# Performance work log

Hardware: AMD Instinct MI355X
Metric: run time of the kernel (lower is better)

The kernel has to match this reference:

```python
import jax, jax.numpy as jnp
import numpy as np

B, C_IN, H, W = 4, 256, 64, 64
LATENT = 256


def setup_inputs() -> dict:
    key = jax.random.key(0)
    ks = jax.random.split(key, 12)
    s_in = 1.0 / np.sqrt(C_IN)
    s_lat = 1.0 / np.sqrt(LATENT)
    return {
        "x": jax.random.normal(ks[0], (B, C_IN, H, W), dtype=jnp.float32),
        # 1x1 conv weights stored as [out, in]
        "wq": jax.random.normal(ks[1], (LATENT, C_IN), dtype=jnp.float32) * s_in,
        "bq": jnp.zeros((LATENT,), dtype=jnp.float32),
        "wk": jax.random.normal(ks[2], (LATENT, C_IN), dtype=jnp.float32) * s_in,
        "bk": jnp.zeros((LATENT,), dtype=jnp.float32),
        "wv": jax.random.normal(ks[3], (LATENT, C_IN), dtype=jnp.float32) * s_in,
        "bv": jnp.zeros((LATENT,), dtype=jnp.float32),
        "w_out": jax.random.normal(ks[4], (C_IN, LATENT), dtype=jnp.float32) * s_lat,
        "b_out": jnp.zeros((C_IN,), dtype=jnp.float32),
        # positional-embedding MLP (torch nn.Linear: y = x @ W.T + b)
        "mlp_w1": jax.random.normal(ks[5], (LATENT, LATENT), dtype=jnp.float32) * s_lat,
        "mlp_b1": jnp.zeros((LATENT,), dtype=jnp.float32),
        "mlp_w2": jax.random.normal(ks[6], (LATENT, LATENT), dtype=jnp.float32) * s_lat,
        "mlp_b2": jnp.zeros((LATENT,), dtype=jnp.float32),
    }


def _sinusoidal_table(timesteps, dim):
    # embed[t, d] = sin(arg) if d even else cos(arg), arg = t / 10000**(2d/dim)
    t = jnp.arange(timesteps, dtype=jnp.float32)[:, None]
    p = jnp.arange(dim, dtype=jnp.float32)[None, :]
    w = t / jnp.power(jnp.float32(10000.0), 2.0 * p / dim)
    even = (jnp.arange(dim) % 2 == 0)[None, :]
    return jnp.where(even, jnp.sin(w), jnp.cos(w))  # [T, dim]


def _conv1x1(x, w, b):
    # x: [B, Cin, H, W], w: [Cout, Cin]
    return jnp.einsum('bchw,oc->bohw', x, w) + b[None, :, None, None]


def reference(x, wq, bq, wk, bk, wv, bv, w_out, b_out, mlp_w1, mlp_b1, mlp_w2, mlp_b2):
    batch, _, h, w_ = x.shape
    L = wq.shape[0]
    hw = h * w_

    q = _conv1x1(x, wq, bq)
    k = _conv1x1(x, wk, bk)
    v = _conv1x1(x, wv, bv)

    pe = _sinusoidal_table(hw, L)                     # [HW, L]
    pe = jax.nn.silu(pe @ mlp_w1.T + mlp_b1) @ mlp_w2.T + mlp_b2
    pe = pe.reshape(1, L, h, w_)                      # faithful to torch reshape

    q = (q + pe).reshape(batch, L, hw)
    k = (k + pe).reshape(batch, L, hw)
    v = (v + pe).reshape(batch, L, hw)

    # attention[b, i, j] = sum_c q[b, c, i] * k[b, c, j] / sqrt(L)
    att = jnp.einsum('bci,bcj->bij', q, k) / jnp.sqrt(jnp.float32(L))
    att = jax.nn.softmax(att, axis=1)                 # SAGAN-style: softmax over queries
    res = jnp.einsum('bci,bij->bcj', v, att)          # bmm(v, attention)
    res = res.reshape(batch, L, h, w_)
    return _conv1x1(res, w_out, b_out)
```

## Files before the change

kernel.cpp:

```cpp
#include <hip/hip_runtime.h>
#include <cstdint>


typedef short s8v __attribute__((ext_vector_type(8)));
typedef float f32x4 __attribute__((ext_vector_type(4)));
typedef unsigned int u32x2 __attribute__((ext_vector_type(2)));
typedef unsigned int u32x4 __attribute__((ext_vector_type(4)));

#define DEVI static __device__ __forceinline__

DEVI unsigned short f2bf(float f) {
  union { float f; uint32_t u; } x; x.f = f;
  uint32_t u = x.u;
  return (unsigned short)((u + 0x7fffu + ((u >> 16) & 1u)) >> 16);
}

DEVI void pl32swap(uint32_t& a, uint32_t& b) {
#if __has_builtin(__builtin_amdgcn_permlane32_swap)
  u32x2 r = __builtin_amdgcn_permlane32_swap(a, b, false, false);
  a = r[0]; b = r[1];
#else
  asm("v_permlane32_swap_b32 %0, %1" : "+v"(a), "+v"(b));
#endif
}

DEVI void gl_lds16(const void* g, void* l) {
  __builtin_amdgcn_global_load_lds(
      (const __attribute__((address_space(1))) void*)g,
      (__attribute__((address_space(3))) void*)l,
      16, 0, 0);
}

DEVI void stage(const unsigned short* src, int ld, unsigned short* lds, int t) {
  gl_lds16(src + (long)(t >> 2) * ld + (t & 3) * 8, lds + (t >> 6) * 512);
}

template <int OBF, int BIAS, int PEM, int SILU>
__global__ __launch_bounds__(256) void gemm_nt(
    const unsigned short* __restrict__ A, const unsigned short* __restrict__ B,
    void* __restrict__ Cp, int K, int N, int ld, long sA, long sB, long sC,
    const float* __restrict__ bias, const float* __restrict__ pe, float scale) {
  const int bz = blockIdx.z;
  const unsigned short* Ab = A + (long)bz * sA;
  const unsigned short* Bb = B + (long)bz * sB;
  const int m0 = blockIdx.x * 128, n0 = blockIdx.y * 128;
  __shared__ __align__(16) unsigned short As[4096], Bs[4096];
  const int t = threadIdx.x;
  const int wave = t >> 6, lane = t & 63;
  const int wr = wave >> 1, wc = wave & 1;

  f32x4 acc[4][4];
#pragma unroll
  for (int i = 0; i < 4; i++)
#pragma unroll
    for (int j = 0; j < 4; j++) acc[i][j] = f32x4{0.f, 0.f, 0.f, 0.f};

  const int rl = lane & 15, kp = (lane >> 4) * 8;

  for (int k0 = 0; k0 < K; k0 += 32) {
    stage(Ab + (long)m0 * ld + k0, ld, As, t);
    stage(Ab + (long)(m0 + 64) * ld + k0, ld, As + 2048, t);
    stage(Bb + (long)n0 * ld + k0, ld, Bs, t);
    stage(Bb + (long)(n0 + 64) * ld + k0, ld, Bs + 2048, t);
    __syncthreads();

    s8v af[4], bfr[4];
#pragma unroll
    for (int i = 0; i < 4; i++)
      af[i] = *(const s8v*)(As + (wr * 64 + i * 16 + rl) * 32 + kp);
#pragma unroll
    for (int j = 0; j < 4; j++)
      bfr[j] = *(const s8v*)(Bs + (wc * 64 + j * 16 + rl) * 32 + kp);
#pragma unroll
    for (int i = 0; i < 4; i++)
#pragma unroll
      for (int j = 0; j < 4; j++)
        acc[i][j] = __builtin_amdgcn_mfma_f32_16x16x32_bf16(af[i], bfr[j],
                                                            acc[i][j], 0, 0, 0);
    __syncthreads();
  }

  const long cb = (long)bz * sC;
#pragma unroll
  for (int i = 0; i < 4; i++) {
    const int r0 = m0 + wr * 64 + i * 16 + (lane >> 4) * 4;
#pragma unroll
    for (int j = 0; j < 4; j++) {
      const int col = n0 + wc * 64 + j * 16 + (lane & 15);
#pragma unroll
      for (int r = 0; r < 4; r++) {
        const int row = r0 + r;
        float val = acc[i][j][r] * scale;
        if (BIAS == 1) val += bias[row];
        if (BIAS == 2) val += bias[col];
        if (PEM == 1) val += pe[(long)row * 4096 + col];
        if (PEM == 2) val += pe[(long)col * 4096 + row];
        if (SILU) val = val / (1.0f + __expf(-val));
        const long ci = cb + (long)row * N + col;
        if (OBF)
          ((unsigned short*)Cp)[ci] = f2bf(val);
        else
          ((float*)Cp)[ci] = val;
      }
    }
  }
}

__global__ __launch_bounds__(256) void gemm_qk(
    const unsigned short* __restrict__ XT, const unsigned short* __restrict__ wqb,
    const unsigned short* __restrict__ wkb, unsigned short* __restrict__ qT,
    unsigned short* __restrict__ kT, const float* __restrict__ bq,
    const float* __restrict__ bk, const float* __restrict__ pe) {
  const int bz = blockIdx.z;
  const unsigned short* Ab = XT + (long)bz * 1048576;
  const int m0 = blockIdx.x * 128, n0 = blockIdx.y * 128;
  __shared__ __align__(16) unsigned short As[4096], Bq[4096], Bk[4096];
  const int t = threadIdx.x;
  const int wave = t >> 6, lane = t & 63;
  const int wr = wave >> 1, wc = wave & 1;

  f32x4 aq[4][4], ak[4][4];
#pragma unroll
  for (int i = 0; i < 4; i++)
#pragma unroll
    for (int j = 0; j < 4; j++) {
      aq[i][j] = f32x4{0.f, 0.f, 0.f, 0.f};
      ak[i][j] = f32x4{0.f, 0.f, 0.f, 0.f};
    }

  const int rl = lane & 15, kp = (lane >> 4) * 8;

  for (int k0 = 0; k0 < 256; k0 += 32) {
    stage(Ab + (long)m0 * 256 + k0, 256, As, t);
    stage(Ab + (long)(m0 + 64) * 256 + k0, 256, As + 2048, t);
    stage(wqb + (long)n0 * 256 + k0, 256, Bq, t);
    stage(wqb + (long)(n0 + 64) * 256 + k0, 256, Bq + 2048, t);
    stage(wkb + (long)n0 * 256 + k0, 256, Bk, t);
    stage(wkb + (long)(n0 + 64) * 256 + k0, 256, Bk + 2048, t);
    __syncthreads();

    s8v af[4], bq4[4], bk4[4];
#pragma unroll
    for (int i = 0; i < 4; i++)
      af[i] = *(const s8v*)(As + (wr * 64 + i * 16 + rl) * 32 + kp);
#pragma unroll
    for (int j = 0; j < 4; j++) {
      bq4[j] = *(const s8v*)(Bq + (wc * 64 + j * 16 + rl) * 32 + kp);
      bk4[j] = *(const s8v*)(Bk + (wc * 64 + j * 16 + rl) * 32 + kp);
    }
#pragma unroll
    for (int i = 0; i < 4; i++)
#pragma unroll
      for (int j = 0; j < 4; j++) {
        aq[i][j] = __builtin_amdgcn_mfma_f32_16x16x32_bf16(af[i], bq4[j],
                                                           aq[i][j], 0, 0, 0);
        ak[i][j] = __builtin_amdgcn_mfma_f32_16x16x32_bf16(af[i], bk4[j],
                                                           ak[i][j], 0, 0, 0);
      }
    __syncthreads();
  }

  const long cb = (long)bz * 1048576;
#pragma unroll
  for (int i = 0; i < 4; i++) {
    const int r0 = m0 + wr * 64 + i * 16 + (lane >> 4) * 4;
#pragma unroll
    for (int j = 0; j < 4; j++) {
      const int col = n0 + wc * 64 + j * 16 + (lane & 15);
#pragma unroll
      for (int r = 0; r < 4; r++) {
        const int row = r0 + r;
        const float p = pe[(long)col * 4096 + row];
        qT[cb + (long)row * 256 + col] = f2bf(aq[i][j][r] + bq[col] + p);
        kT[cb + (long)row * 256 + col] = f2bf(ak[i][j][r] + bk[col] + p);
      }
    }
  }
}

__global__ __launch_bounds__(512, 2) void flash_attn(
    const unsigned short* __restrict__ qTp, const unsigned short* __restrict__ kTp,
    const unsigned short* __restrict__ vBp, float* __restrict__ oPart,
    float* __restrict__ lPart) {
  const int bid = blockIdx.x;
  const int xcd = bid & 7;
  const int b = xcd >> 1, ihalf = xcd & 1;
  const int j0 = (bid >> 3) * 128;
  const long S = 1048576;
  const long ibase = (long)ihalf * 2048;
  const unsigned short* q = qTp + (long)b * S;
  const unsigned short* k = kTp + (long)b * S;
  const unsigned short* v = vBp + (long)b * S;
  const int ob = b * 2 + ihalf;

  __shared__ __align__(16) unsigned char ldsb[131584];

  const int t = threadIdx.x;
  const int wave = t >> 6, lane = t & 63;
  const int jq = wave & 3, ch = wave >> 2;
  const int rl = lane & 15, g = lane >> 4;
  const int kp = g * 8;
  const int ksw = ((g ^ ((rl >> 1) & 3)) << 3);
  const int qrow = (rl & 3) | ((rl & 4) << 1) | ((rl & 8) >> 1);
  const int kswq = ((g ^ ((qrow >> 1) & 3)) << 3);
  const int th = t >> 8, tt = t & 255;

  const unsigned short* krow = k + (long)(j0 + jq * 32 + rl) * 256 + kp;
  s8v kreg[2][8];
#pragma unroll
  for (int jf = 0; jf < 2; jf++)
#pragma unroll
    for (int s = 0; s < 8; s++)
      kreg[jf][s] = *(const s8v*)(krow + jf * 16 * 256 + s * 32);

  f32x4 oacc[16][2];
#pragma unroll
  for (int cf = 0; cf < 16; cf++)
#pragma unroll
    for (int jf = 0; jf < 2; jf++) oacc[cf][jf] = f32x4{0.f, 0.f, 0.f, 0.f};
  float plsum[2] = {0.f, 0.f};

  const int tr = tt >> 2, tc = tt & 3;
  const int sc = (tc ^ ((tr >> 1) & 3)) * 8;
  const unsigned short* qsrc[4];
  const unsigned short* vsrc[4];
  const int dsto = (tt >> 6) * 512;
#pragma unroll
  for (int ss = 0; ss < 4; ss++) {
    const int s_ = ss * 2 + th;
    qsrc[ss] = q + ibase * 256 + s_ * 32 + (long)tr * 256 + sc;
    vsrc[ss] = v + (long)((s_ >> 1) * 64) * 4096 + ibase + (s_ & 1) * 32 +
               (long)tr * 4096 + sc;
  }

#define STAGE_QV(bufsel)                                                     \
  {                                                                          \
    unsigned short* qD = (unsigned short*)(ldsb + ((bufsel) << 15));         \
    unsigned short* vD = (unsigned short*)(ldsb + 65536 + ((bufsel) << 15)); \
    _Pragma("unroll") for (int ss = 0; ss < 4; ss++) {                       \
      const int s_ = ss * 2 + th;                                            \
      gl_lds16(qsrc[ss], qD + s_ * 2048 + dsto);                             \
      gl_lds16(vsrc[ss], vD + s_ * 2048 + dsto);                             \
      qsrc[ss] += 16384;                     \
      vsrc[ss] += 64;                        \
    }                                                                        \
  }

  STAGE_QV(0)

  for (int n = 0; n < 32; ++n) {
    const int cur = n & 1;
    __syncthreads();
    STAGE_QV(cur ^ 1)

    f32x4 sa[2][2];
#pragma unroll
    for (int kk = 0; kk < 2; kk++)
#pragma unroll
      for (int jf = 0; jf < 2; jf++) sa[kk][jf] = f32x4{0.f, 0.f, 0.f, 0.f};
    const unsigned short* qbase =
        (const unsigned short*)(ldsb + (cur << 15)) +
        (ch * 32 + qrow) * 32 + kswq;
#pragma unroll
    for (int s = 0; s < 8; s++) {
      s8v qf0 = *(const s8v*)(qbase + s * 2048);
      s8v qf1 = *(const s8v*)(qbase + s * 2048 + 512);
      sa[0][0] = __builtin_amdgcn_mfma_f32_16x16x32_bf16(qf0, kreg[0][s],
                                                         sa[0][0], 0, 0, 0);
      sa[0][1] = __builtin_amdgcn_mfma_f32_16x16x32_bf16(qf0, kreg[1][s],
                                                         sa[0][1], 0, 0, 0);
      sa[1][0] = __builtin_amdgcn_mfma_f32_16x16x32_bf16(qf1, kreg[0][s],
                                                         sa[1][0], 0, 0, 0);
      sa[1][1] = __builtin_amdgcn_mfma_f32_16x16x32_bf16(qf1, kreg[1][s],
                                                         sa[1][1], 0, 0, 0);
    }

    uint32_t pd[2][2][2];
#pragma unroll
    for (int kk = 0; kk < 2; kk++)
#pragma unroll
      for (int jf = 0; jf < 2; jf++) {
        const float p0 = exp2f(sa[kk][jf][0] * 0.09016844005556021f);
        const float p1 = exp2f(sa[kk][jf][1] * 0.09016844005556021f);
        const float p2 = exp2f(sa[kk][jf][2] * 0.09016844005556021f);
        const float p3 = exp2f(sa[kk][jf][3] * 0.09016844005556021f);
        plsum[jf] += (p0 + p1) + (p2 + p3);
        pd[kk][jf][0] = (uint32_t)f2bf(p0) | ((uint32_t)f2bf(p1) << 16);
        pd[kk][jf][1] = (uint32_t)f2bf(p2) | ((uint32_t)f2bf(p3) << 16);
      }

    s8v pB[2];
#pragma unroll
    for (int jf = 0; jf < 2; jf++) {
      uint32_t a0 = pd[0][jf][0], b0 = pd[1][jf][0];
      uint32_t a1 = pd[0][jf][1], b1 = pd[1][jf][1];
      pl32swap(a0, b0);
      pl32swap(a1, b1);
      u32x4 w4 = {a0, a1, b0, b1};
      pB[jf] = __builtin_bit_cast(s8v, w4);
    }

    const unsigned short* vbase =
        (const unsigned short*)(ldsb + 65536 + (cur << 15)) + ch * 2048 +
        rl * 32 + ksw;
#pragma unroll
    for (int cf = 0; cf < 16; cf++) {
      s8v vb = *(const s8v*)(vbase + (cf >> 2) * 4096 + (cf & 3) * 512);
      oacc[cf][0] = __builtin_amdgcn_mfma_f32_16x16x32_bf16(vb, pB[0],
                                                            oacc[cf][0], 0, 0, 0);
      oacc[cf][1] = __builtin_amdgcn_mfma_f32_16x16x32_bf16(vb, pB[1],
                                                            oacc[cf][1], 0, 0, 0);
    }
  }

#pragma unroll
  for (int jf = 0; jf < 2; jf++) {
    plsum[jf] += __shfl_xor(plsum[jf], 16);
    plsum[jf] += __shfl_xor(plsum[jf], 32);
  }

  __syncthreads();
  float4* ex = (float4*)ldsb;
  float* exl = (float*)(ldsb + 131072);
  if (ch == 1) {
#pragma unroll
    for (int jf = 0; jf < 2; jf++) {
#pragma unroll
      for (int cf = 0; cf < 16; cf++)
        ex[jq * 2048 + (jf * 16 + rl) * 64 + cf * 4 + g] =
            float4{oacc[cf][jf][0], oacc[cf][jf][1], oacc[cf][jf][2],
                   oacc[cf][jf][3]};
      if (g == 0) exl[jq * 32 + jf * 16 + rl] = plsum[jf];
    }
  }
  __syncthreads();
  if (ch == 0) {
    float4* op4 = (float4*)(oPart + (long)ob * 1048576);
#pragma unroll
    for (int jf = 0; jf < 2; jf++) {
      const int jl = jq * 32 + jf * 16 + rl;
      if (g == 0)
        lPart[(long)ob * 4096 + j0 + jl] = plsum[jf] + exl[jl];
#pragma unroll
      for (int cf = 0; cf < 16; cf++) {
        const float4 o = ex[jq * 2048 + (jf * 16 + rl) * 64 + cf * 4 + g];
        op4[(long)(j0 + jl) * 64 + cf * 4 + g] =
            float4{oacc[cf][jf][0] + o.x, oacc[cf][jf][1] + o.y,
                   oacc[cf][jf][2] + o.z, oacc[cf][jf][3] + o.w};
      }
    }
  }
#undef STAGE_QV
}

__global__ __launch_bounds__(256) void combine_o(
    const float* __restrict__ oPart, const float* __restrict__ lPart,
    unsigned short* __restrict__ rT) {
  const long idx = (long)blockIdx.x * 256 + threadIdx.x;
  const int c4 = idx & 63;
  const int j = (idx >> 6) & 4095;
  const int b = idx >> 18;
  const long p0 = ((long)(b * 2) * 1048576 + (long)j * 256) / 4 + c4;
  const float4 a = ((const float4*)oPart)[p0];
  const float4 d = ((const float4*)oPart)[p0 + 262144];
  const float l = lPart[(long)(b * 2) * 4096 + j] +
                  lPart[(long)(b * 2 + 1) * 4096 + j];
  const float inv = 1.0f / l;
  ushort4 o;
  o.x = f2bf((a.x + d.x) * inv);
  o.y = f2bf((a.y + d.y) * inv);
  o.z = f2bf((a.z + d.z) * inv);
  o.w = f2bf((a.w + d.w) * inv);
  ((ushort4*)rT)[(long)b * 262144 + (long)j * 64 + c4] = o;
}

__global__ __launch_bounds__(256) void convert6(
    const float* __restrict__ a0, const float* __restrict__ a1,
    const float* __restrict__ a2, const float* __restrict__ a3,
    const float* __restrict__ a4, const float* __restrict__ a5,
    unsigned short* __restrict__ dst) {
  int idx = blockIdx.x * 256 + threadIdx.x;
  int m = idx >> 16, r = idx & 65535;
  const float* s;
  switch (m) {
    case 0: s = a0; break;
    case 1: s = a1; break;
    case 2: s = a2; break;
    case 3: s = a3; break;
    case 4: s = a4; break;
    default: s = a5; break;
  }
  dst[idx] = f2bf(s[r]);
}

__global__ __launch_bounds__(256) void embed_k(unsigned short* __restrict__ e) {
  int idx = blockIdx.x * 256 + threadIdx.x;
  int t = idx >> 8, d = idx & 255;
  float freq = powf(10000.0f, -(float)d * (1.0f / 128.0f));
  float w = (float)t * freq;
  float r = (d & 1) ? cosf(w) : sinf(w);
  e[idx] = f2bf(r);
}

__global__ void transpose_x(const float* __restrict__ x,
                            unsigned short* __restrict__ xt) {
  __shared__ float tile[32][33];
  const int b = blockIdx.z;
  const int s0 = blockIdx.x * 32, c0 = blockIdx.y * 32;
  const int tx = threadIdx.x, ty = threadIdx.y;
  const float* xb = x + (long)b * 256 * 4096;
#pragma unroll
  for (int r = 0; r < 32; r += 8)
    tile[ty + r][tx] = xb[(long)(c0 + ty + r) * 4096 + s0 + tx];
  __syncthreads();
  unsigned short* xtb = xt + (long)b * 4096 * 256;
#pragma unroll
  for (int r = 0; r < 32; r += 8)
    xtb[(long)(s0 + ty + r) * 256 + c0 + tx] = f2bf(tile[tx][ty + r]);
}

extern "C" void kernel_launch(void* const* d_in, const int* in_sizes, int n_in,
                              void* d_out, int out_size, void* d_ws,
                              size_t ws_size, hipStream_t stream) {
  const float* x  = (const float*)d_in[0];
  const float* wq = (const float*)d_in[1];
  const float* bq = (const float*)d_in[2];
  const float* wk = (const float*)d_in[3];
  const float* bk = (const float*)d_in[4];
  const float* wv = (const float*)d_in[5];
  const float* bv = (const float*)d_in[6];
  const float* wo = (const float*)d_in[7];
  const float* bo = (const float*)d_in[8];
  const float* w1 = (const float*)d_in[9];
  const float* b1 = (const float*)d_in[10];
  const float* w2 = (const float*)d_in[11];
  const float* b2 = (const float*)d_in[12];
  float* out = (float*)d_out;

  char* ws = (char*)d_ws;
  unsigned short* wqb = (unsigned short*)(ws + 0);
  unsigned short* wkb = (unsigned short*)(ws + 131072);
  unsigned short* wvb = (unsigned short*)(ws + 262144);
  unsigned short* wob = (unsigned short*)(ws + 393216);
  unsigned short* w1b = (unsigned short*)(ws + 524288);
  unsigned short* w2b = (unsigned short*)(ws + 655360);
  unsigned short* emb = (unsigned short*)(ws + 786432);
  unsigned short* h1b = (unsigned short*)(ws + 2883584);
  float*          peF = (float*)(ws + 4980736);
  unsigned short* XT  = (unsigned short*)(ws + 9175040);
  unsigned short* qT  = (unsigned short*)(ws + 17563648);
  unsigned short* kT  = (unsigned short*)(ws + 25952256);
  unsigned short* vB  = (unsigned short*)(ws + 34340864);
  unsigned short* rT  = (unsigned short*)(ws + 42729472);
  float*          oP  = (float*)(ws + 51118080);
  float*          lP  = (float*)(ws + 84672512);
  (void)ws_size; (void)in_sizes; (void)n_in; (void)out_size;

  const dim3 B256(256);
  const long S = 1048576;

  convert6<<<1536, B256, 0, stream>>>(wq, wk, wv, wo, w1, w2, wqb);
  embed_k<<<4096, B256, 0, stream>>>(emb);
  gemm_nt<1, 2, 0, 1><<<dim3(32, 2, 1), B256, 0, stream>>>(
      emb, w1b, h1b, 256, 256, 256, 0, 0, 0, b1, nullptr, 1.0f);
  gemm_nt<0, 2, 0, 0><<<dim3(32, 2, 1), B256, 0, stream>>>(
      h1b, w2b, peF, 256, 256, 256, 0, 0, 0, b2, nullptr, 1.0f);
  transpose_x<<<dim3(128, 8, 4), dim3(32, 8), 0, stream>>>(x, XT);
  gemm_qk<<<dim3(32, 2, 4), B256, 0, stream>>>(XT, wqb, wkb, qT, kT, bq, bk,
                                               peF);
  gemm_nt<1, 1, 1, 0><<<dim3(2, 32, 4), B256, 0, stream>>>(
      wvb, XT, vB, 256, 4096, 256, 0, S, S, bv, peF, 1.0f);

  flash_attn<<<256, dim3(512), 0, stream>>>(qT, kT, vB, oP, lP);
  combine_o<<<4096, B256, 0, stream>>>(oP, lP, rT);

  gemm_nt<0, 1, 0, 0><<<dim3(2, 32, 4), B256, 0, stream>>>(
      wob, rT, out, 256, 4096, 256, 0, S, S, bo, nullptr, 1.0f);
}
```

Measured before the change: 167.2 us.

## Fuse split-softmax combine into output projection GEMM and cheapen embedding math

Removes the separate combine_o kernel and the bf16 rT intermediate. The output 1x1-conv GEMM now reads the two fp32 partial attention outputs and their row sums directly, normalises them, converts to bf16 and writes its B tile to LDS. The sinusoidal embedding kernel also swaps powf/sinf/cosf for exp2f and __sincosf. In exchange, each GEMM block re-reads fp32 partials (twice the bytes of bf16) with no double buffering, and the fast sincos loses accuracy for large arguments.

```diff
diff --git a/kernel.cpp b/kernel.cpp
--- a/kernel.cpp
+++ b/kernel.cpp
@@ -178,6 +178,89 @@
   }
 }
 
+__global__ __launch_bounds__(256) void gemm_out_f(
+    const unsigned short* __restrict__ wob, const float* __restrict__ oPart,
+    const float* __restrict__ lPart, const float* __restrict__ bo,
+    float* __restrict__ out) {
+  const int bz = blockIdx.z;
+  const int m0 = blockIdx.x * 128, n0 = blockIdx.y * 128;
+  __shared__ __align__(16) unsigned short As[4096], Bs[4096];
+  const int t = threadIdx.x;
+  const int wave = t >> 6, lane = t & 63;
+  const int wr = wave >> 1, wc = wave & 1;
+
+  f32x4 acc[4][4];
+#pragma unroll
+  for (int i = 0; i < 4; i++)
+#pragma unroll
+    for (int j = 0; j < 4; j++) acc[i][j] = f32x4{0.f, 0.f, 0.f, 0.f};
+
+  const int rl = lane & 15, kp = (lane >> 4) * 8;
+  const int tr = t >> 2, tc8 = (t & 3) * 8;
+
+  const int j0_ = n0 + tr, j1_ = n0 + 64 + tr;
+  const float* l0p = lPart + (long)(bz * 2) * 4096;
+  const float* l1p = lPart + (long)(bz * 2 + 1) * 4096;
+  const float inv0 = 1.0f / (l0p[j0_] + l1p[j0_]);
+  const float inv1 = 1.0f / (l0p[j1_] + l1p[j1_]);
+  const float* oP0 = oPart + (long)(bz * 2) * 1048576;
+  const float* oP1 = oPart + (long)(bz * 2 + 1) * 1048576;
+
+  for (int k0 = 0; k0 < 256; k0 += 32) {
+    stage(wob + (long)m0 * 256 + k0, 256, As, t);
+    stage(wob + (long)(m0 + 64) * 256 + k0, 256, As + 2048, t);
+#pragma unroll
+    for (int h = 0; h < 2; h++) {
+      const int j = h ? j1_ : j0_;
+      const float inv = h ? inv1 : inv0;
+      const float4* a4 = (const float4*)(oP0 + (long)j * 256 + k0 + tc8);
+      const float4* d4 = (const float4*)(oP1 + (long)j * 256 + k0 + tc8);
+      const float4 a0 = a4[0], a1 = a4[1], d0 = d4[0], d1 = d4[1];
+      s8v pk;
+      pk[0] = (short)f2bf((a0.x + d0.x) * inv);
+      pk[1] = (short)f2bf((a0.y + d0.y) * inv);
+      pk[2] = (short)f2bf((a0.z + d0.z) * inv);
+      pk[3] = (short)f2bf((a0.w + d0.w) * inv);
+      pk[4] = (short)f2bf((a1.x + d1.x) * inv);
+      pk[5] = (short)f2bf((a1.y + d1.y) * inv);
+      pk[6] = (short)f2bf((a1.z + d1.z) * inv);
+      pk[7] = (short)f2bf((a1.w + d1.w) * inv);
+      *(s8v*)(Bs + h * 2048 + tr * 32 + tc8) = pk;
+    }
+    __syncthreads();
+
+    s8v af[4], bfr[4];
+#pragma unroll
+    for (int i = 0; i < 4; i++)
+      af[i] = *(const s8v*)(As + (wr * 64 + i * 16 + rl) * 32 + kp);
+#pragma unroll
+    for (int j = 0; j < 4; j++)
+      bfr[j] = *(const s8v*)(Bs + (wc * 64 + j * 16 + rl) * 32 + kp);
+#pragma unroll
+    for (int i = 0; i < 4; i++)
+#pragma unroll
+      for (int j = 0; j < 4; j++)
+        acc[i][j] = __builtin_amdgcn_mfma_f32_16x16x32_bf16(af[i], bfr[j],
+                                                            acc[i][j], 0, 0, 0);
+    __syncthreads();
+  }
+
+  const long cb = (long)bz * 1048576;
+#pragma unroll
+  for (int i = 0; i < 4; i++) {
+    const int r0 = m0 + wr * 64 + i * 16 + (lane >> 4) * 4;
+#pragma unroll
+    for (int j = 0; j < 4; j++) {
+      const int col = n0 + wc * 64 + j * 16 + (lane & 15);
+#pragma unroll
+      for (int r = 0; r < 4; r++) {
+        const int row = r0 + r;
+        out[cb + (long)row * 4096 + col] = acc[i][j][r] + bo[row];
+      }
+    }
+  }
+}
+
 __global__ __launch_bounds__(512, 2) void flash_attn(
     const unsigned short* __restrict__ qTp, const unsigned short* __restrict__ kTp,
     const unsigned short* __restrict__ vBp, float* __restrict__ oPart,
@@ -241,8 +324,8 @@
       const int s_ = ss * 2 + th;                                            \
       gl_lds16(qsrc[ss], qD + s_ * 2048 + dsto);                             \
       gl_lds16(vsrc[ss], vD + s_ * 2048 + dsto);                             \
-      qsrc[ss] += 16384;                     \
-      vsrc[ss] += 64;                        \
+      qsrc[ss] += 16384;                                                     \
+      vsrc[ss] += 64;                                                        \
     }                                                                        \
   }
 
@@ -351,27 +434,6 @@
     }
   }
 #undef STAGE_QV
-}
-
-__global__ __launch_bounds__(256) void combine_o(
-    const float* __restrict__ oPart, const float* __restrict__ lPart,
-    unsigned short* __restrict__ rT) {
-  const long idx = (long)blockIdx.x * 256 + threadIdx.x;
-  const int c4 = idx & 63;
-  const int j = (idx >> 6) & 4095;
-  const int b = idx >> 18;
-  const long p0 = ((long)(b * 2) * 1048576 + (long)j * 256) / 4 + c4;
-  const float4 a = ((const float4*)oPart)[p0];
-  const float4 d = ((const float4*)oPart)[p0 + 262144];
-  const float l = lPart[(long)(b * 2) * 4096 + j] +
-                  lPart[(long)(b * 2 + 1) * 4096 + j];
-  const float inv = 1.0f / l;
-  ushort4 o;
-  o.x = f2bf((a.x + d.x) * inv);
-  o.y = f2bf((a.y + d.y) * inv);
-  o.z = f2bf((a.z + d.z) * inv);
-  o.w = f2bf((a.w + d.w) * inv);
-  ((ushort4*)rT)[(long)b * 262144 + (long)j * 64 + c4] = o;
 }
 
 __global__ __launch_bounds__(256) void convert6(
@@ -396,10 +458,11 @@
 __global__ __launch_bounds__(256) void embed_k(unsigned short* __restrict__ e) {
   int idx = blockIdx.x * 256 + threadIdx.x;
   int t = idx >> 8, d = idx & 255;
-  float freq = powf(10000.0f, -(float)d * (1.0f / 128.0f));
+  float freq = exp2f((float)d * -0.10381025296573598f);
   float w = (float)t * freq;
-  float r = (d & 1) ? cosf(w) : sinf(w);
-  e[idx] = f2bf(r);
+  float s, c;
+  __sincosf(w, &s, &c);
+  e[idx] = f2bf((d & 1) ? c : s);
 }
 
 __global__ void transpose_x(const float* __restrict__ x,
@@ -451,7 +514,6 @@
   unsigned short* qT  = (unsigned short*)(ws + 17563648);
   unsigned short* kT  = (unsigned short*)(ws + 25952256);
   unsigned short* vB  = (unsigned short*)(ws + 34340864);
-  unsigned short* rT  = (unsigned short*)(ws + 42729472);
   float*          oP  = (float*)(ws + 51118080);
   float*          lP  = (float*)(ws + 84672512);
   (void)ws_size; (void)in_sizes; (void)n_in; (void)out_size;
@@ -472,8 +534,6 @@
       wvb, XT, vB, 256, 4096, 256, 0, S, S, bv, peF, 1.0f);
 
   flash_attn<<<256, dim3(512), 0, stream>>>(qT, kT, vB, oP, lP);
-  combine_o<<<4096, B256, 0, stream>>>(oP, lP, rT);
-
-  gemm_nt<0, 1, 0, 0><<<dim3(2, 32, 4), B256, 0, stream>>>(
-      wob, rT, out, 256, 4096, 256, 0, S, S, bo, nullptr, 1.0f);
-}
+
+  gemm_out_f<<<dim3(2, 32, 4), B256, 0, stream>>>(wob, oP, lP, bo, out);
+}
```

Measured after the change: 162.0 us. 1.03x faster.
